# Optimization experiments

Hardware: AMD Instinct MI355X
Metric: run time of the kernel (lower is better)

## Reference

```python
import jax, jax.numpy as jnp
import numpy as np

EMB = 256
HID = 1024
N_TRACKS = 4096
SEQ = 9
SCALE = 4.0


def setup_inputs() -> dict:
    key = jax.random.key(0)
    ks = jax.random.split(key, 12)

    def init(k, shape, fan_in):
        b = 1.0 / np.sqrt(fan_in)
        return jax.random.uniform(k, shape, jnp.float32, -b, b)

    return {
        "observed": jax.random.normal(ks[0], (SEQ, N_TRACKS, 2), jnp.float32),
        "emb_w": init(ks[1], (EMB - 2, 2), 2),
        "emb_b": init(ks[2], (EMB - 2,), 2),
        "enc_wih": init(ks[3], (4 * HID, EMB), HID),
        "enc_whh": init(ks[4], (4 * HID, HID), HID),
        "enc_b": init(ks[5], (4 * HID,), HID),
        "dec_wih": init(ks[6], (4 * HID, EMB), HID),
        "dec_whh": init(ks[7], (4 * HID, HID), HID),
        "dec_b": init(ks[8], (4 * HID,), HID),
        "h2n_w": init(ks[9], (5, HID), HID),
        "h2n_b": init(ks[10], (5,), HID),
        "n_predict": 12,
    }


def _forward(observed, emb_w, emb_b, enc_wih, enc_whh, enc_b,
             dec_wih, dec_whh, dec_b, h2n_w, h2n_b, n_predict):
    n = observed.shape[1]
    H = enc_whh.shape[1]
    E = enc_wih.shape[1]

    def cell(x, h, c, wih, whh, b):
        # PyTorch LSTMCell gate order: i, f, g, o
        g = x @ wih.T + h @ whh.T + b
        i, f, gg, o = jnp.split(g, 4, axis=-1)
        c = jax.nn.sigmoid(f) * c + jax.nn.sigmoid(i) * jnp.tanh(gg)
        h = jax.nn.sigmoid(o) * jnp.tanh(c)
        return h, c

    def embed(v):
        # Linear(2, E-2) -> ReLU, then 2 zero tag channels
        e = jax.nn.relu((v * SCALE) @ emb_w.T + emb_b)
        return jnp.concatenate([e, jnp.zeros((v.shape[0], 2), e.dtype)], axis=1)

    def h2n(h):
        raw = h @ h2n_w.T + h2n_b
        sig = 0.01 + 0.2 * jax.nn.sigmoid(raw[:, 2:4])  # sigma1, sigma2
        rho = 0.7 * jax.nn.sigmoid(raw[:, 4:5])          # rho
        return jnp.concatenate([raw[:, :2], sig, rho], axis=1)

    def step(params, h, c, obs1, obs2):
        wih, whh, b = params
        mask = ~(jnp.isnan(obs1[:, 0]) | jnp.isnan(obs2[:, 0]))  # [N]
        x = embed(obs2 - obs1)
        h2, c2 = cell(x, h, c, wih, whh, b)
        nrm = h2n(h2)
        m = mask[:, None]
        h = jnp.where(m, h2, h)
        c = jnp.where(m, c2, c)
        normal = jnp.where(m, nrm, jnp.nan)
        pos = obs2 + normal[:, :2]
        return h, c, normal, pos

    h = jnp.zeros((n, H), observed.dtype)
    c = jnp.zeros((n, H), observed.dtype)

    # encoder start tag
    tag_enc = jnp.zeros((n, E), observed.dtype).at[:, -2].set(1.0)
    h, c = cell(tag_enc, h, c, enc_wih, enc_whh, enc_b)

    enc_p = (enc_wih, enc_whh, enc_b)

    def enc_scan(carry, obs_pair):
        h, c = carry
        o1, o2 = obs_pair
        h, c, normal, pos = step(enc_p, h, c, o1, o2)
        return (h, c), (normal, pos)

    (h, c), (enc_normals, enc_positions) = jax.lax.scan(
        enc_scan, (h, c), (observed[:-1], observed[1:]))

    # decoder start tag
    tag_dec = jnp.zeros((n, E), observed.dtype).at[:, -1].set(1.0)
    h, c = cell(tag_dec, h, c, dec_wih, dec_whh, dec_b)

    dec_p = (dec_wih, dec_whh, dec_b)
    p1, p2 = enc_positions[-2], enc_positions[-1]

    def dec_scan(carry, _):
        h, c, p1, p2 = carry
        o1 = jax.lax.stop_gradient(p1)  # .detach() in torch
        o2 = jax.lax.stop_gradient(p2)
        h, c, normal, pos = step(dec_p, h, c, o1, o2)
        return (h, c, p2, pos), (normal, pos)

    _, (dec_normals, dec_positions) = jax.lax.scan(
        dec_scan, (h, c, p1, p2), None, length=n_predict - 1)

    rel_pred_scene = jnp.concatenate([enc_normals, dec_normals], axis=0)
    pred_scene = jnp.concatenate([enc_positions, dec_positions], axis=0)
    return rel_pred_scene, pred_scene


def reference(observed, emb_w, emb_b, enc_wih, enc_whh, enc_b,
              dec_wih, dec_whh, dec_b, h2n_w, h2n_b, n_predict):
    return _forward(observed, emb_w, emb_b, enc_wih, enc_whh, enc_b,
                    dec_wih, dec_whh, dec_b, h2n_w, h2n_b, n_predict)
```

## Files before the change

### kernel.cpp

```cpp
#include <hip/hip_runtime.h>
#include <stdint.h>

#define NTRK 4096
#define HIDN 1024
#define EMBN 256
#define KTOT 1280
#define NOUT 19

typedef __attribute__((ext_vector_type(8))) short short8;
typedef __attribute__((ext_vector_type(4))) float f32x4;

typedef __attribute__((address_space(1))) const void GV;
typedef __attribute__((address_space(3))) void LV;

__device__ __forceinline__ uint16_t f2bf(float f) {
  uint32_t u = __float_as_uint(f);
  u += 0x7fffu + ((u >> 16) & 1u);
  return (uint16_t)(u >> 16);
}
__device__ __forceinline__ float bf2f(uint16_t v) {
  return __uint_as_float(((uint32_t)v) << 16);
}
__device__ __forceinline__ float sigm(float x) { return 1.0f / (1.0f + expf(-x)); }
__device__ __forceinline__ float sigmf_(float x) {
  return __builtin_amdgcn_rcpf(1.0f + __expf(-x));
}
__device__ __forceinline__ float tanhf_(float x) {
  return 2.0f * __builtin_amdgcn_rcpf(1.0f + __expf(-2.0f * x)) - 1.0f;
}

__global__ __launch_bounds__(256) void prep_weights(
    const float* __restrict__ encWih, const float* __restrict__ encWhh,
    const float* __restrict__ encB,
    const float* __restrict__ decWih, const float* __restrict__ decWhh,
    const float* __restrict__ decB,
    uint16_t* __restrict__ WcatE, uint16_t* __restrict__ WcatD,
    float* __restrict__ biasE, float* __restrict__ biasD, float* __restrict__ biasDT)
{
  const int jp = blockIdx.x;
  const int q = jp >> 6, r = jp & 63;
  const int gate = r >> 4, l16 = r & 15;
  const int u = q * 16 + l16;
  const int orig = gate * 1024 + u;
  const int t = threadIdx.x;

  WcatE[(size_t)jp * KTOT + t] = f2bf(encWih[(size_t)orig * 256 + t]);
  WcatD[(size_t)jp * KTOT + t] = f2bf(decWih[(size_t)orig * 256 + t]);
#pragma unroll
  for (int c = 0; c < 4; c++) {
    WcatE[(size_t)jp * KTOT + 256 + c * 256 + t] = f2bf(encWhh[(size_t)orig * 1024 + c * 256 + t]);
    WcatD[(size_t)jp * KTOT + 256 + c * 256 + t] = f2bf(decWhh[(size_t)orig * 1024 + c * 256 + t]);
  }
  if (t == 0) {
    biasE[jp]  = encB[orig];
    biasD[jp]  = decB[orig];
    biasDT[jp] = decB[orig] + decWih[(size_t)orig * 256 + 255];
  }
}

__global__ void init_h0(const float* __restrict__ encWih, const float* __restrict__ encB,
                        float* __restrict__ h0, float* __restrict__ c0)
{
  const int u = blockIdx.x * 256 + threadIdx.x;
  if (u >= 1024) return;
  const float gi = encWih[(size_t)(u) * 256 + 254]        + encB[u];
  const float gg = encWih[(size_t)(2048 + u) * 256 + 254] + encB[2048 + u];
  const float go = encWih[(size_t)(3072 + u) * 256 + 254] + encB[3072 + u];
  const float c = sigm(gi) * tanhf(gg);
  c0[u] = c;
  h0[u] = sigm(go) * tanhf(c);
}

__global__ __launch_bounds__(256) void bias_h0(
    const float* __restrict__ encWhh, const float* __restrict__ encB,
    const float* __restrict__ h0, float* __restrict__ biasE0)
{
  const int jp = blockIdx.x * 4 + (threadIdx.x >> 6);
  const int lane = threadIdx.x & 63;
  const int q = jp >> 6, r = jp & 63;
  const int gate = r >> 4, l16 = r & 15;
  const int orig = gate * 1024 + (q * 16 + l16);
  const float* wr = encWhh + (size_t)orig * 1024 + lane * 16;
  const float* hr = h0 + lane * 16;
  float s = 0.f;
#pragma unroll
  for (int e = 0; e < 16; e++) s += wr[e] * hr[e];
  s += __shfl_xor(s, 32); s += __shfl_xor(s, 16); s += __shfl_xor(s, 8);
  s += __shfl_xor(s, 4);  s += __shfl_xor(s, 2);  s += __shfl_xor(s, 1);
  if (lane == 0) biasE0[jp] = encB[orig] + s;
}

__global__ __launch_bounds__(256) void embed_k(
    const float* __restrict__ o1, const float* __restrict__ o2,
    const float* __restrict__ ew, const float* __restrict__ eb,
    uint16_t* __restrict__ X)
{
  const int trk = blockIdx.x;
  const int j = threadIdx.x;
  const float vx = (o2[trk * 2]     - o1[trk * 2])     * 4.0f;
  const float vy = (o2[trk * 2 + 1] - o1[trk * 2 + 1]) * 4.0f;
  float e = 0.f;
  if (j < 254) e = fmaxf(vx * ew[j * 2] + vy * ew[j * 2 + 1] + eb[j], 0.f);
  X[(size_t)trk * 256 + j] = f2bf(e);
}

__global__ __launch_bounds__(256) void embed8(
    const float* __restrict__ observed, const float* __restrict__ ew,
    const float* __restrict__ eb, uint16_t* __restrict__ Xall)
{
  const int t = blockIdx.y;
  const int trk = blockIdx.x;
  const int j = threadIdx.x;
  const float* o1 = observed + ((size_t)t * 4096 + trk) * 2;
  const float* o2 = o1 + 4096 * 2;
  const float vx = (o2[0] - o1[0]) * 4.0f;
  const float vy = (o2[1] - o1[1]) * 4.0f;
  float e = 0.f;
  if (j < 254) e = fmaxf(vx * ew[j * 2] + vy * ew[j * 2 + 1] + eb[j], 0.f);
  Xall[((size_t)t * 4096 + trk) * 256 + j] = f2bf(e);
}

__global__ __launch_bounds__(512, 4) void gemm_lstm(
    const uint16_t* __restrict__ X,    const uint16_t* __restrict__ Hin,
    const uint16_t* __restrict__ Wcat, const float* __restrict__ bias,
    float* __restrict__ Cst,           uint16_t* __restrict__ Hout,
    const float* __restrict__ obs1,    const float* __restrict__ obs2,
    const float* __restrict__ h0v,     const float* __restrict__ c0v,
    int k0, int kend, int maskmode, int initmode)
{
  __shared__ uint16_t As[3 * 4096];
  __shared__ uint16_t Bs[3 * 8192];
  __shared__ uint8_t  smask[128];

  const int tid  = threadIdx.x;
  const int w    = tid >> 6;
  const int lane = tid & 63;
  const int wr   = w >> 2;
  const int wc   = w & 3;
  const int quad = lane >> 4;
  const int l15  = lane & 15;

  const int bid = blockIdx.y * 16 + blockIdx.x;
  const int xcd = bid & 7;
  const int j   = bid >> 3;
  const int bmS = (xcd >> 2) * 16 + (j >> 2);
  const int bnS = (xcd & 3) * 4 + (j & 3);
  const int bm  = bmS * 128;
  const int bn  = bnS * 256;

  const int NT = (kend - k0) >> 5;

  if (tid < 128) {
    bool m = true;
    if (maskmode) {
      const float a = obs1[(bm + tid) * 2];
      const float b = obs2[(bm + tid) * 2];
      m = !((a != a) || (b != b));
    }
    smask[tid] = m ? 1 : 0;
  }

  const int srow = w * 16 + (lane >> 2);
  const int sch  = ((lane & 3) ^ ((lane >> 3) & 3)) * 8;
  const uint16_t* pXr = X ? X + (size_t)(bm + srow) * 256 + sch : (const uint16_t*)0;
  const uint16_t* pHr = Hin  + (size_t)(bm + srow) * 1024 + sch;
  const uint16_t* pWr = Wcat + (size_t)(bn + srow) * (size_t)KTOT + sch;

  auto stage = [&](int V, int slot) {
    if (V >= NT) return;
    const int kg = k0 + V * 32;
    uint16_t* ad = As + slot * 4096 + w * 16 * 32;
    if (kg < 256) {
      __builtin_amdgcn_global_load_lds((GV*)(pXr + kg),         (LV*)ad, 16, 0, 0);
    } else {
      __builtin_amdgcn_global_load_lds((GV*)(pHr + (kg - 256)), (LV*)ad, 16, 0, 0);
    }
    uint16_t* bd = Bs + slot * 8192 + w * 16 * 32;
    __builtin_amdgcn_global_load_lds((GV*)(pWr + kg),                        (LV*)bd,          16, 0, 0);
    __builtin_amdgcn_global_load_lds((GV*)(pWr + (size_t)128 * KTOT + kg),   (LV*)(bd + 4096), 16, 0, 0);
  };

  f32x4 acc[4][4];
#pragma unroll
  for (int i = 0; i < 4; i++)
#pragma unroll
    for (int n = 0; n < 4; n++) acc[i][n] = (f32x4){0.f, 0.f, 0.f, 0.f};

  stage(0, 0); stage(1, 1);
  asm volatile("s_waitcnt vmcnt(3)" ::: "memory");
  __builtin_amdgcn_s_barrier();

  const int cc = (quad ^ ((l15 >> 1) & 3)) * 8;

  int sT = 0;
  for (int T = 0; T < NT; T++) {
    const int sS = (sT == 0) ? 2 : sT - 1;
    const uint16_t* Ab = As + sT * 4096;
    const uint16_t* Bb = Bs + sT * 8192;
    short8 a[4], b[4];
#pragma unroll
    for (int i = 0; i < 4; i++)
      a[i] = *(const short8*)(Ab + (wr * 64 + i * 16 + l15) * 32 + cc);
#pragma unroll
    for (int n = 0; n < 4; n++)
      b[n] = *(const short8*)(Bb + (wc * 64 + n * 16 + l15) * 32 + cc);
    stage(T + 2, sS);
    __builtin_amdgcn_s_setprio(1);
#pragma unroll
    for (int i = 0; i < 4; i++)
#pragma unroll
      for (int n = 0; n < 4; n++)
        acc[i][n] = __builtin_amdgcn_mfma_f32_16x16x32_bf16(a[i], b[n], acc[i][n], 0, 0, 0);
    __builtin_amdgcn_s_setprio(0);
    if (T < NT - 2) {
      asm volatile("s_waitcnt vmcnt(3)" ::: "memory");
    } else {
      asm volatile("s_waitcnt vmcnt(0)" ::: "memory");
    }
    __builtin_amdgcn_s_barrier();
    sT = (sT == 2) ? 0 : sT + 1;
  }

  const int u  = ((bn >> 6) + wc) * 16 + l15;
  const int jb = bn + wc * 64 + l15;
  const float b_i = bias[jb];
  const float b_f = bias[jb + 16];
  const float b_g = bias[jb + 32];
  const float b_o = bias[jb + 48];
  const float c0u = initmode ? c0v[u] : 0.f;
  const uint16_t h0u = initmode ? f2bf(h0v[u]) : (uint16_t)0;

#pragma unroll
  for (int i = 0; i < 4; i++) {
#pragma unroll
    for (int r = 0; r < 4; r++) {
      const int row = bm + wr * 64 + i * 16 + quad * 4 + r;
      const size_t idx = (size_t)row * 1024 + u;
      uint16_t hv;
      if (smask[row - bm]) {
        const float cprev = initmode ? c0u : Cst[idx];
        const float gi = acc[i][0][r] + b_i;
        const float gf = acc[i][1][r] + b_f;
        const float gg = acc[i][2][r] + b_g;
        const float go = acc[i][3][r] + b_o;
        const float cn = sigmf_(gf) * cprev + sigmf_(gi) * tanhf_(gg);
        Cst[idx] = cn;
        hv = f2bf(sigmf_(go) * tanhf_(cn));
      } else if (initmode) {
        Cst[idx] = c0u;
        hv = h0u;
      } else {
        hv = Hin[idx];
      }
      Hout[idx] = hv;
    }
  }
}

__global__ __launch_bounds__(256) void h2n_pos(
    const uint16_t* __restrict__ H, const float* __restrict__ w5, const float* __restrict__ b5,
    const float* __restrict__ obs1, const float* __restrict__ obs2,
    float* __restrict__ outrel, float* __restrict__ outpos,
    const float* __restrict__ pprev, const float* __restrict__ ew,
    const float* __restrict__ eb, uint16_t* __restrict__ Xnext, int do_embed)
{
  const int lane  = threadIdx.x & 63;
  const int track = blockIdx.x * 4 + (threadIdx.x >> 6);

  const uint16_t* hrow = H + (size_t)track * 1024 + lane * 16;
  const short8 v0 = *(const short8*)(hrow);
  const short8 v1 = *(const short8*)(hrow + 8);
  float hv[16];
#pragma unroll
  for (int j = 0; j < 8; j++) {
    hv[j]     = bf2f((uint16_t)v0[j]);
    hv[8 + j] = bf2f((uint16_t)v1[j]);
  }
  const int kb = lane * 16;
  float p[5];
#pragma unroll
  for (int o = 0; o < 5; o++) {
    const float* wr = w5 + (size_t)o * 1024 + kb;
    float s = 0.f;
#pragma unroll
    for (int j = 0; j < 16; j++) s += hv[j] * wr[j];
    p[o] = s;
  }
#pragma unroll
  for (int o = 0; o < 5; o++) {
    float v = p[o];
    v += __shfl_xor(v, 32); v += __shfl_xor(v, 16); v += __shfl_xor(v, 8);
    v += __shfl_xor(v, 4);  v += __shfl_xor(v, 2);  v += __shfl_xor(v, 1);
    p[o] = v;
  }
  const float o1x = obs1[track * 2];
  const float o2x = obs2[track * 2];
  const float o2y = obs2[track * 2 + 1];
  const bool msk = !((o1x != o1x) || (o2x != o2x));
  float n0 = p[0] + b5[0];
  float n1 = p[1] + b5[1];
  float n2 = 0.01f + 0.2f * sigmf_(p[2] + b5[2]);
  float n3 = 0.01f + 0.2f * sigmf_(p[3] + b5[3]);
  float n4 = 0.7f  * sigmf_(p[4] + b5[4]);
  if (!msk) {
    const float qn = __uint_as_float(0x7fc00000u);
    n0 = n1 = n2 = n3 = n4 = qn;
  }
  const float posx = o2x + n0;
  const float posy = o2y + n1;
  if (lane == 0) {
    float* rr = outrel + (size_t)track * 5;
    rr[0] = n0; rr[1] = n1; rr[2] = n2; rr[3] = n3; rr[4] = n4;
    outpos[track * 2]     = posx;
    outpos[track * 2 + 1] = posy;
  }
  if (do_embed) {
    const float vx = (posx - pprev[track * 2])     * 4.0f;
    const float vy = (posy - pprev[track * 2 + 1]) * 4.0f;
    uint16_t* xr = Xnext + (size_t)track * 256;
#pragma unroll
    for (int ii = 0; ii < 4; ii++) {
      const int j = ii * 64 + lane;
      float e = 0.f;
      if (j < 254) e = fmaxf(vx * ew[j * 2] + vy * ew[j * 2 + 1] + eb[j], 0.f);
      xr[j] = f2bf(e);
    }
  }
}

extern "C" void kernel_launch(void* const* d_in, const int* in_sizes, int n_in,
                              void* d_out, int out_size, void* d_ws, size_t ws_size,
                              hipStream_t stream)
{
  const float* observed = (const float*)d_in[0];
  const float* emb_w    = (const float*)d_in[1];
  const float* emb_b    = (const float*)d_in[2];
  const float* enc_wih  = (const float*)d_in[3];
  const float* enc_whh  = (const float*)d_in[4];
  const float* enc_b    = (const float*)d_in[5];
  const float* dec_wih  = (const float*)d_in[6];
  const float* dec_whh  = (const float*)d_in[7];
  const float* dec_b    = (const float*)d_in[8];
  const float* h2n_w    = (const float*)d_in[9];
  const float* h2n_b    = (const float*)d_in[10];

  char* ws = (char*)d_ws;
  size_t off = 0;
  auto alloc = [&](size_t bytes) -> void* {
    size_t cur = (off + 255) & ~(size_t)255;
    off = cur + bytes;
    return (void*)(ws + cur);
  };
  uint16_t* WcatE = (uint16_t*)alloc((size_t)4096 * KTOT * 2);
  uint16_t* WcatD = (uint16_t*)alloc((size_t)4096 * KTOT * 2);
  float*    biasE = (float*)alloc(4096 * 4);
  float*    biasE0= (float*)alloc(4096 * 4);
  float*    biasD = (float*)alloc(4096 * 4);
  float*    biasDT= (float*)alloc(4096 * 4);
  float*    h0    = (float*)alloc(1024 * 4);
  float*    c0    = (float*)alloc(1024 * 4);
  uint16_t* HA    = (uint16_t*)alloc((size_t)4096 * 1024 * 2);
  uint16_t* HB    = (uint16_t*)alloc((size_t)4096 * 1024 * 2);
  float*    Cst   = (float*)alloc((size_t)4096 * 1024 * 4);
  uint16_t* Xb    = (uint16_t*)alloc((size_t)4096 * 256 * 2);
  const size_t xall_bytes = (size_t)8 * 4096 * 256 * 2;
  const bool use_xall = (off + 256 + xall_bytes) <= ws_size;
  uint16_t* Xall = use_xall ? (uint16_t*)alloc(xall_bytes) : nullptr;

  float* outrel = (float*)d_out;
  float* outpos = outrel + (size_t)NOUT * 4096 * 5;

  prep_weights<<<4096, 256, 0, stream>>>(enc_wih, enc_whh, enc_b, dec_wih, dec_whh, dec_b,
                                         WcatE, WcatD, biasE, biasD, biasDT);
  init_h0<<<4, 256, 0, stream>>>(enc_wih, enc_b, h0, c0);
  bias_h0<<<1024, 256, 0, stream>>>(enc_whh, enc_b, h0, biasE0);
  if (use_xall) {
    embed8<<<dim3(4096, 8), 256, 0, stream>>>(observed, emb_w, emb_b, Xall);
  }

  uint16_t* Hin = HA;
  uint16_t* Hout = HB;
  const dim3 ggrid(16, 32);

  for (int t = 0; t < 8; t++) {
    const float* o1 = observed + (size_t)t * 4096 * 2;
    const float* o2 = observed + (size_t)(t + 1) * 4096 * 2;
    uint16_t* Xt = Xb;
    if (use_xall) {
      Xt = Xall + (size_t)t * 4096 * 256;
    } else {
      embed_k<<<4096, 256, 0, stream>>>(o1, o2, emb_w, emb_b, Xb);
    }
    if (t == 0) {
      gemm_lstm<<<ggrid, 512, 0, stream>>>(Xt, Hin, WcatE, biasE0, Cst, Hout, o1, o2,
                                           h0, c0, 0, 256, 1, 1);
    } else {
      gemm_lstm<<<ggrid, 512, 0, stream>>>(Xt, Hin, WcatE, biasE, Cst, Hout, o1, o2,
                                           nullptr, nullptr, 0, KTOT, 1, 0);
    }
    const int de = (t == 7) ? 1 : 0;
    h2n_pos<<<1024, 256, 0, stream>>>(Hout, h2n_w, h2n_b, o1, o2,
                                      outrel + (size_t)t * 4096 * 5,
                                      outpos + (size_t)t * 4096 * 2,
                                      outpos + (size_t)6 * 4096 * 2, emb_w, emb_b, Xb, de);
    uint16_t* tmp = Hin; Hin = Hout; Hout = tmp;
  }

  gemm_lstm<<<ggrid, 512, 0, stream>>>(nullptr, Hin, WcatD, biasDT, Cst, Hout,
                                       nullptr, nullptr, nullptr, nullptr, 256, KTOT, 0, 0);
  { uint16_t* tmp = Hin; Hin = Hout; Hout = tmp; }

  for (int s = 0; s < 11; s++) {
    const float* p1 = outpos + (size_t)(6 + s) * 4096 * 2;
    const float* p2 = outpos + (size_t)(7 + s) * 4096 * 2;
    gemm_lstm<<<ggrid, 512, 0, stream>>>(Xb, Hin, WcatD, biasD, Cst, Hout, p1, p2,
                                         nullptr, nullptr, 0, KTOT, 1, 0);
    const int de = (s < 10) ? 1 : 0;
    h2n_pos<<<1024, 256, 0, stream>>>(Hout, h2n_w, h2n_b, p1, p2,
                                      outrel + (size_t)(8 + s) * 4096 * 5,
                                      outpos + (size_t)(8 + s) * 4096 * 2,
                                      p2, emb_w, emb_b, Xb, de);
    uint16_t* tmp = Hin; Hin = Hout; Hout = tmp;
  }
}
```

Baseline: 1.236 ms.

## Fold encoder h2n head into next-step GEMM launch as extra blocks

In the encoder, the per-step h2n_pos launch is removed. Its work for step t-1 now runs as extra blocks (blockIdx.y >= 32) inside the step-t gemm_lstm launch, reading the previous H buffer. The decoder-start GEMM likewise absorbs the last encoder h2n and the first decoder embedding. This cuts kernel launches and serialization points in the encoder phase, at the cost of more kernel arguments and a bigger grid whose extra light blocks share the GPU with the GEMM blocks.

```diff
diff --git a/kernel.cpp b/kernel.cpp
--- a/kernel.cpp
+++ b/kernel.cpp
@@ -120,19 +120,104 @@
   Xall[((size_t)t * 4096 + trk) * 256 + j] = f2bf(e);
 }
 
+__device__ __forceinline__ void h2n_body(
+    int track, int lane,
+    const uint16_t* __restrict__ H, const float* __restrict__ w5, const float* __restrict__ b5,
+    const float* __restrict__ obs1, const float* __restrict__ obs2,
+    float* __restrict__ outrel, float* __restrict__ outpos,
+    const float* __restrict__ pprev, const float* __restrict__ ew,
+    const float* __restrict__ eb, uint16_t* __restrict__ Xnext, int do_embed)
+{
+  const uint16_t* hrow = H + (size_t)track * 1024 + lane * 16;
+  const short8 v0 = *(const short8*)(hrow);
+  const short8 v1 = *(const short8*)(hrow + 8);
+  float hv[16];
+#pragma unroll
+  for (int j = 0; j < 8; j++) {
+    hv[j]     = bf2f((uint16_t)v0[j]);
+    hv[8 + j] = bf2f((uint16_t)v1[j]);
+  }
+  const int kb = lane * 16;
+  float p[5];
+#pragma unroll
+  for (int o = 0; o < 5; o++) {
+    const float* wr = w5 + (size_t)o * 1024 + kb;
+    float s = 0.f;
+#pragma unroll
+    for (int j = 0; j < 16; j++) s += hv[j] * wr[j];
+    p[o] = s;
+  }
+#pragma unroll
+  for (int o = 0; o < 5; o++) {
+    float v = p[o];
+    v += __shfl_xor(v, 32); v += __shfl_xor(v, 16); v += __shfl_xor(v, 8);
+    v += __shfl_xor(v, 4);  v += __shfl_xor(v, 2);  v += __shfl_xor(v, 1);
+    p[o] = v;
+  }
+  const float o1x = obs1[track * 2];
+  const float o2x = obs2[track * 2];
+  const float o2y = obs2[track * 2 + 1];
+  const bool msk = !((o1x != o1x) || (o2x != o2x));
+  float n0 = p[0] + b5[0];
+  float n1 = p[1] + b5[1];
+  float n2 = 0.01f + 0.2f * sigmf_(p[2] + b5[2]);
+  float n3 = 0.01f + 0.2f * sigmf_(p[3] + b5[3]);
+  float n4 = 0.7f  * sigmf_(p[4] + b5[4]);
+  if (!msk) {
+    const float qn = __uint_as_float(0x7fc00000u);
+    n0 = n1 = n2 = n3 = n4 = qn;
+  }
+  const float posx = o2x + n0;
+  const float posy = o2y + n1;
+  if (lane == 0) {
+    float* rr = outrel + (size_t)track * 5;
+    rr[0] = n0; rr[1] = n1; rr[2] = n2; rr[3] = n3; rr[4] = n4;
+    outpos[track * 2]     = posx;
+    outpos[track * 2 + 1] = posy;
+  }
+  if (do_embed) {
+    const float vx = (posx - pprev[track * 2])     * 4.0f;
+    const float vy = (posy - pprev[track * 2 + 1]) * 4.0f;
+    uint16_t* xr = Xnext + (size_t)track * 256;
+#pragma unroll
+    for (int ii = 0; ii < 4; ii++) {
+      const int j = ii * 64 + lane;
+      float e = 0.f;
+      if (j < 254) e = fmaxf(vx * ew[j * 2] + vy * ew[j * 2 + 1] + eb[j], 0.f);
+      xr[j] = f2bf(e);
+    }
+  }
+}
+
 __global__ __launch_bounds__(512, 4) void gemm_lstm(
     const uint16_t* __restrict__ X,    const uint16_t* __restrict__ Hin,
     const uint16_t* __restrict__ Wcat, const float* __restrict__ bias,
     float* __restrict__ Cst,           uint16_t* __restrict__ Hout,
     const float* __restrict__ obs1,    const float* __restrict__ obs2,
     const float* __restrict__ h0v,     const float* __restrict__ c0v,
-    int k0, int kend, int maskmode, int initmode)
+    int k0, int kend, int maskmode, int initmode,
+    const uint16_t* __restrict__ phH,  const float* __restrict__ w5,
+    const float* __restrict__ b5,
+    const float* __restrict__ ph_o1,   const float* __restrict__ ph_o2,
+    float* __restrict__ ph_rel,        float* __restrict__ ph_pos,
+    const float* __restrict__ ph_prev, const float* __restrict__ ew,
+    const float* __restrict__ eb,      uint16_t* __restrict__ ph_Xn,
+    int ph_embed)
 {
   __shared__ uint16_t As[3 * 4096];
   __shared__ uint16_t Bs[3 * 8192];
   __shared__ uint8_t  smask[128];
 
   const int tid  = threadIdx.x;
+
+  if (blockIdx.y >= 32) {
+    const int pb = (blockIdx.y - 32) * 16 + blockIdx.x;
+    const int track = pb * 8 + (tid >> 6);
+    h2n_body(track, tid & 63, phH, w5, b5, ph_o1, ph_o2,
+             ph_rel, ph_pos, ph_prev, ew, eb, ph_Xn, ph_embed);
+    return;
+  }
+
   const int w    = tid >> 6;
   const int lane = tid & 63;
   const int wr   = w >> 2;
@@ -266,66 +351,8 @@
 {
   const int lane  = threadIdx.x & 63;
   const int track = blockIdx.x * 4 + (threadIdx.x >> 6);
-
-  const uint16_t* hrow = H + (size_t)track * 1024 + lane * 16;
-  const short8 v0 = *(const short8*)(hrow);
-  const short8 v1 = *(const short8*)(hrow + 8);
-  float hv[16];
-#pragma unroll
-  for (int j = 0; j < 8; j++) {
-    hv[j]     = bf2f((uint16_t)v0[j]);
-    hv[8 + j] = bf2f((uint16_t)v1[j]);
-  }
-  const int kb = lane * 16;
-  float p[5];
-#pragma unroll
-  for (int o = 0; o < 5; o++) {
-    const float* wr = w5 + (size_t)o * 1024 + kb;
-    float s = 0.f;
-#pragma unroll
-    for (int j = 0; j < 16; j++) s += hv[j] * wr[j];
-    p[o] = s;
-  }
-#pragma unroll
-  for (int o = 0; o < 5; o++) {
-    float v = p[o];
-    v += __shfl_xor(v, 32); v += __shfl_xor(v, 16); v += __shfl_xor(v, 8);
-    v += __shfl_xor(v, 4);  v += __shfl_xor(v, 2);  v += __shfl_xor(v, 1);
-    p[o] = v;
-  }
-  const float o1x = obs1[track * 2];
-  const float o2x = obs2[track * 2];
-  const float o2y = obs2[track * 2 + 1];
-  const bool msk = !((o1x != o1x) || (o2x != o2x));
-  float n0 = p[0] + b5[0];
-  float n1 = p[1] + b5[1];
-  float n2 = 0.01f + 0.2f * sigmf_(p[2] + b5[2]);
-  float n3 = 0.01f + 0.2f * sigmf_(p[3] + b5[3]);
-  float n4 = 0.7f  * sigmf_(p[4] + b5[4]);
-  if (!msk) {
-    const float qn = __uint_as_float(0x7fc00000u);
-    n0 = n1 = n2 = n3 = n4 = qn;
-  }
-  const float posx = o2x + n0;
-  const float posy = o2y + n1;
-  if (lane == 0) {
-    float* rr = outrel + (size_t)track * 5;
-    rr[0] = n0; rr[1] = n1; rr[2] = n2; rr[3] = n3; rr[4] = n4;
-    outpos[track * 2]     = posx;
-    outpos[track * 2 + 1] = posy;
-  }
-  if (do_embed) {
-    const float vx = (posx - pprev[track * 2])     * 4.0f;
-    const float vy = (posy - pprev[track * 2 + 1]) * 4.0f;
-    uint16_t* xr = Xnext + (size_t)track * 256;
-#pragma unroll
-    for (int ii = 0; ii < 4; ii++) {
-      const int j = ii * 64 + lane;
-      float e = 0.f;
-      if (j < 254) e = fmaxf(vx * ew[j * 2] + vy * ew[j * 2 + 1] + eb[j], 0.f);
-      xr[j] = f2bf(e);
-    }
-  }
+  h2n_body(track, lane, H, w5, b5, obs1, obs2, outrel, outpos,
+           pprev, ew, eb, Xnext, do_embed);
 }
 
 extern "C" void kernel_launch(void* const* d_in, const int* in_sizes, int n_in,
@@ -381,6 +408,7 @@
   uint16_t* Hin = HA;
   uint16_t* Hout = HB;
   const dim3 ggrid(16, 32);
+  const dim3 pgrid(16, 64);
 
   for (int t = 0; t < 8; t++) {
     const float* o1 = observed + (size_t)t * 4096 * 2;
@@ -393,28 +421,42 @@
     }
     if (t == 0) {
       gemm_lstm<<<ggrid, 512, 0, stream>>>(Xt, Hin, WcatE, biasE0, Cst, Hout, o1, o2,
-                                           h0, c0, 0, 256, 1, 1);
+                                           h0, c0, 0, 256, 1, 1,
+                                           nullptr, nullptr, nullptr, nullptr, nullptr,
+                                           nullptr, nullptr, nullptr, nullptr, nullptr,
+                                           nullptr, 0);
     } else {
-      gemm_lstm<<<ggrid, 512, 0, stream>>>(Xt, Hin, WcatE, biasE, Cst, Hout, o1, o2,
-                                           nullptr, nullptr, 0, KTOT, 1, 0);
-    }
-    const int de = (t == 7) ? 1 : 0;
-    h2n_pos<<<1024, 256, 0, stream>>>(Hout, h2n_w, h2n_b, o1, o2,
-                                      outrel + (size_t)t * 4096 * 5,
-                                      outpos + (size_t)t * 4096 * 2,
-                                      outpos + (size_t)6 * 4096 * 2, emb_w, emb_b, Xb, de);
+      const float* po1 = observed + (size_t)(t - 1) * 4096 * 2;
+      const float* po2 = observed + (size_t)t * 4096 * 2;
+      gemm_lstm<<<pgrid, 512, 0, stream>>>(Xt, Hin, WcatE, biasE, Cst, Hout, o1, o2,
+                                           nullptr, nullptr, 0, KTOT, 1, 0,
+                                           Hin, h2n_w, h2n_b, po1, po2,
+                                           outrel + (size_t)(t - 1) * 4096 * 5,
+                                           outpos + (size_t)(t - 1) * 4096 * 2,
+                                           nullptr, emb_w, emb_b, nullptr, 0);
+    }
     uint16_t* tmp = Hin; Hin = Hout; Hout = tmp;
   }
 
-  gemm_lstm<<<ggrid, 512, 0, stream>>>(nullptr, Hin, WcatD, biasDT, Cst, Hout,
-                                       nullptr, nullptr, nullptr, nullptr, 256, KTOT, 0, 0);
+  gemm_lstm<<<pgrid, 512, 0, stream>>>(nullptr, Hin, WcatD, biasDT, Cst, Hout,
+                                       nullptr, nullptr, nullptr, nullptr, 256, KTOT, 0, 0,
+                                       Hin, h2n_w, h2n_b,
+                                       observed + (size_t)7 * 4096 * 2,
+                                       observed + (size_t)8 * 4096 * 2,
+                                       outrel + (size_t)7 * 4096 * 5,
+                                       outpos + (size_t)7 * 4096 * 2,
+                                       outpos + (size_t)6 * 4096 * 2,
+                                       emb_w, emb_b, Xb, 1);
   { uint16_t* tmp = Hin; Hin = Hout; Hout = tmp; }
 
   for (int s = 0; s < 11; s++) {
     const float* p1 = outpos + (size_t)(6 + s) * 4096 * 2;
     const float* p2 = outpos + (size_t)(7 + s) * 4096 * 2;
     gemm_lstm<<<ggrid, 512, 0, stream>>>(Xb, Hin, WcatD, biasD, Cst, Hout, p1, p2,
-                                         nullptr, nullptr, 0, KTOT, 1, 0);
+                                         nullptr, nullptr, 0, KTOT, 1, 0,
+                                         nullptr, nullptr, nullptr, nullptr, nullptr,
+                                         nullptr, nullptr, nullptr, nullptr, nullptr,
+                                         nullptr, 0);
     const int de = (s < 10) ? 1 : 0;
     h2n_pos<<<1024, 256, 0, stream>>>(Hout, h2n_w, h2n_b, p1, p2,
                                       outrel + (size_t)(8 + s) * 4096 * 5,
```

Measured after the change: 1.203 ms (median of 2 runs). 2.7% less time.
